# Kernel optimization log

Hardware: AMD Instinct MI355X
Metric: run time of the kernel (lower is better)

Reference implementation:

```python
import jax, jax.numpy as jnp
import numpy as np

H = 8  # n_heads from init_kwargs
EPS = 1e-5


def _ln(x, g, b):
    m = jnp.mean(x, axis=-1, keepdims=True)
    v = jnp.mean((x - m) ** 2, axis=-1, keepdims=True)
    return (x - m) * jax.lax.rsqrt(v + EPS) * g + b


def setup_inputs() -> dict:
    key = jax.random.key(0)
    B, d_m, n, L, p_d = 1, 256, 128, 1024, 128
    ks = jax.random.split(key, 12)
    s = 0.02
    return {
        "msa": jax.random.normal(ks[0], (B, d_m, n, L), jnp.float32),
        "pairs": jax.random.normal(ks[1], (B, n, n, p_d), jnp.float32),
        "ln_m_g": jnp.ones((d_m,), jnp.float32),
        "ln_m_b": jnp.zeros((d_m,), jnp.float32),
        "ln_p_g": jnp.ones((p_d,), jnp.float32),
        "ln_p_b": jnp.zeros((p_d,), jnp.float32),
        "Wq": jax.random.normal(ks[2], (d_m, d_m), jnp.float32) * s,
        "Wk": jax.random.normal(ks[3], (d_m, d_m), jnp.float32) * s,
        "Wv": jax.random.normal(ks[4], (d_m, d_m), jnp.float32) * s,
        "Wg": jax.random.normal(ks[5], (d_m, d_m), jnp.float32) * s,
        "bg": jnp.zeros((d_m,), jnp.float32),
        "Wb": jax.random.normal(ks[6], (p_d, H), jnp.float32) * s,
        "Wo": jax.random.normal(ks[7], (d_m, d_m), jnp.float32) * s,
        "bo": jnp.zeros((d_m,), jnp.float32),
    }


def reference(msa, pairs, ln_m_g, ln_m_b, ln_p_g, ln_p_b,
              Wq, Wk, Wv, Wg, bg, Wb, Wo, bo):
    B, d_m, n, L = msa.shape
    dh = d_m // H
    sqrt_c = jnp.sqrt(jnp.asarray(dh, msa.dtype))

    x = _ln(jnp.transpose(msa, (0, 3, 2, 1)), ln_m_g, ln_m_b)      # [B,L,n,d_m]
    p = _ln(pairs, ln_p_g, ln_p_b)                                   # [B,n,n,p_d]

    # pair bias: (B,n,n,H) -> (B,1,H,n_q,n_k)
    bias = jnp.transpose(jnp.einsum('bijc,ch->bijh', p, Wb), (0, 3, 1, 2))[:, None]

    def heads(y):  # [B,L,n,d_m] -> [B,L,H,n,dh]
        return jnp.transpose(y.reshape(B, L, n, H, dh), (0, 1, 3, 2, 4))

    q = heads(x @ Wq)
    k = heads(x @ Wk)
    v = heads(x @ Wv)
    g = jax.nn.sigmoid(heads(x @ Wg + bg))

    scores = jnp.einsum('blhnd,blhmd->blhnm', q, k) / sqrt_c + bias  # [B,L,H,n,n]
    w = jax.nn.softmax(scores, axis=-1)
    attn = g * jnp.einsum('blhnm,blhmd->blhnd', w, v)                # [B,L,H,n,dh]

    attn = jnp.transpose(attn, (0, 1, 3, 2, 4)).reshape(B, L, n, d_m)
    out = attn @ Wo + bo                                             # [B,L,n,d_m]
    return jnp.transpose(out, (0, 3, 2, 1))                          # [B,d_m,n,L]
```

## Files before the change

### kernel.cpp

```cpp
#include <hip/hip_runtime.h>

__device__ __forceinline__ float bf1(unsigned short s){ return __uint_as_float((unsigned)s << 16); }
__device__ __forceinline__ unsigned short f2bf(float f){
  unsigned u = __float_as_uint(f);
  u += 0x7fffu + ((u >> 16) & 1u);
  return (unsigned short)(u >> 16);
}
__device__ __forceinline__ unsigned cvt_pk_bf16(float a, float b){
  unsigned r;
  asm("v_cvt_pk_bf16_f32 %0, %1, %2" : "=v"(r) : "v"(a), "v"(b));
  return r;
}

typedef __attribute__((ext_vector_type(8))) short short8;
typedef __attribute__((ext_vector_type(4))) float f32x4;

__device__ __forceinline__ f32x4 mfma16(short8 a, short8 b, f32x4 c){
  return __builtin_amdgcn_mfma_f32_16x16x32_bf16(a, b, c, 0, 0, 0);
}

#define GLOAD_LDS16(g, l) \
  __builtin_amdgcn_global_load_lds((const __attribute__((address_space(1))) unsigned int*)(g), \
                                   (__attribute__((address_space(3))) unsigned int*)(l), 16, 0, 0)

__global__ __launch_bounds__(256) void ln_msa_kernel(
    const float* __restrict__ msa, const float* __restrict__ gam,
    const float* __restrict__ bet, unsigned short* __restrict__ x16)
{
  __shared__ float tile[256*33];
  __shared__ float ps[8*32], pq[8*32];
  __shared__ float mean_s[32], rstd_s[32];
  const int t = threadIdx.x;
  const int l0 = blockIdx.x * 32;
  const int n  = blockIdx.y;
  {
    const int lt = t & 31, ct = t >> 5;
    for (int r = 0; r < 32; ++r) {
      int c = r*8 + ct;
      tile[c*33 + lt] = msa[(size_t)c*131072 + (size_t)n*1024 + l0 + lt];
    }
  }
  __syncthreads();
  {
    const int lt = t & 31, cp = t >> 5;
    float s1 = 0.f, s2 = 0.f;
    for (int cc = 0; cc < 32; ++cc) {
      int c = cp*32 + ((cc + cp*4) & 31);
      float v = tile[c*33 + lt];
      s1 += v; s2 += v*v;
    }
    ps[cp*32 + lt] = s1; pq[cp*32 + lt] = s2;
  }
  __syncthreads();
  if (t < 32) {
    float s1 = 0.f, s2 = 0.f;
    for (int cp = 0; cp < 8; ++cp){ s1 += ps[cp*32+t]; s2 += pq[cp*32+t]; }
    float m = s1 * (1.f/256.f);
    float v = s2 * (1.f/256.f) - m*m;
    mean_s[t] = m;
    rstd_s[t] = rsqrtf(v + 1e-5f);
  }
  __syncthreads();
  {
    const float g = gam[t], b = bet[t];
    for (int l = 0; l < 32; ++l) {
      float v = (tile[t*33 + l] - mean_s[l]) * rstd_s[l] * g + b;
      x16[((size_t)(l0+l)*128 + n)*256 + t] = f2bf(v);
    }
  }
}

__global__ __launch_bounds__(64) void pair_bias_kernel(
    const float* __restrict__ pairs, const float* __restrict__ gam,
    const float* __restrict__ bet, const float* __restrict__ Wb,
    float* __restrict__ biasb)
{
  const int j = blockIdx.x, i = blockIdx.y;
  const int t = threadIdx.x;
  const float* row = pairs + ((size_t)i*128 + j)*128;
  float v0 = row[t], v1 = row[t+64];
  float s = v0 + v1;
  #pragma unroll
  for (int o = 1; o < 64; o <<= 1) s += __shfl_xor(s, o, 64);
  float m = s * (1.f/128.f);
  float d0 = v0 - m, d1 = v1 - m;
  float q = d0*d0 + d1*d1;
  #pragma unroll
  for (int o = 1; o < 64; o <<= 1) q += __shfl_xor(q, o, 64);
  float rstd = rsqrtf(q * (1.f/128.f) + 1e-5f);
  float n0 = d0 * rstd * gam[t]    + bet[t];
  float n1 = d1 * rstd * gam[t+64] + bet[t+64];
  #pragma unroll
  for (int h = 0; h < 8; ++h) {
    float p = n0 * Wb[t*8 + h] + n1 * Wb[(t+64)*8 + h];
    #pragma unroll
    for (int o = 1; o < 64; o <<= 1) p += __shfl_xor(p, o, 64);
    if (t == h) biasb[((size_t)h*128 + i)*128 + j] = p;
  }
}

__global__ __launch_bounds__(256) void wprep_kernel(
    const float* __restrict__ Wq, const float* __restrict__ Wk,
    const float* __restrict__ Wv, const float* __restrict__ Wg,
    const float* __restrict__ Wo,
    unsigned short* __restrict__ Wt, unsigned short* __restrict__ WoT)
{
  const int n = blockIdx.x, k = threadIdx.x;
  if (n < 1024) {
    const int mat = n >> 8, nl = n & 255;
    const float* W = (mat==0) ? Wq : (mat==1) ? Wk : (mat==2) ? Wv : Wg;
    float v = W[(size_t)k*256 + nl];
    if (mat == 0) v *= 0.17677669529663689f;
    Wt[(size_t)n*256 + k] = f2bf(v);
  } else {
    const int c = n - 1024;
    WoT[(size_t)c*256 + k] = f2bf(Wo[(size_t)k*256 + c]);
  }
}

__global__ __launch_bounds__(512) void fused_qkvg_attn(
    const unsigned short* __restrict__ X, const unsigned short* __restrict__ Wt,
    const float* __restrict__ bg, const float* __restrict__ biasb,
    unsigned short* __restrict__ attn2)
{
  __shared__ __align__(16) unsigned short lds[81920];
  unsigned short* Xs  = lds;
  unsigned short* Wst = lds + 32768;
  unsigned short* qs  = lds + 65536;
  unsigned short* ks  = lds + 69632;
  unsigned short* vs  = lds + 73728;
  unsigned short* gs  = lds + 77824;

  const int t = threadIdx.x, l = blockIdx.x;
  const int w = t>>6, fr = t&15, quad = (t>>4)&3;
  const int mat = w>>1, dh = (w&1)*16;
  const int d0 = dh + quad*4;
  unsigned short* pw = Wst + w*2176;
  const int rbase = w*16;
  const f32x4 zero4 = {0.f,0.f,0.f,0.f};

  #pragma unroll
  for (int s = 0; s < 8; ++s) {
    int cid = s*512 + t;
    int k0b = cid>>10, r = (cid>>3)&127, pch = cid&7;
    int c = pch ^ (r&7);
    const unsigned short* g = X + ((size_t)l*128 + r)*256 + k0b*64 + c*8;
    GLOAD_LDS16(g, Xs + (cid & ~63)*8);
  }

  for (int h = 0; h < 8; ++h) {
    #pragma unroll
    for (int s = 0; s < 8; ++s) {
      int cid = s*512 + t;
      int k0b = cid>>10, r = (cid>>3)&127, pch = cid&7;
      int c = pch ^ (r&7);
      const unsigned short* g = Wt + ((size_t)((r>>5)*256 + h*32 + (r&31)))*256 + k0b*64 + c*8;
      GLOAD_LDS16(g, Wst + (cid & ~63)*8);
    }
    __syncthreads();

    f32x4 acc[8] = {};
    for (int k0 = 0; k0 < 4; ++k0) {
      #pragma unroll
      for (int kt = 0; kt < 2; ++kt) {
        const int ck = kt*4 + quad;
        const int lr = mat*32 + dh + fr;
        short8 bf = *(const short8*)(Wst + k0*8192 + lr*64 + (ck^(lr&7))*8);
        #pragma unroll
        for (int mt = 0; mt < 8; ++mt) {
          const int r = mt*16 + fr;
          short8 af = *(const short8*)(Xs + k0*8192 + r*64 + (ck^(r&7))*8);
          acc[mt] = mfma16(bf, af, acc[mt]);
        }
      }
    }

    if (mat == 2) {
      #pragma unroll
      for (int mt = 0; mt < 8; ++mt) {
        const int m = mt*16 + fr;
        #pragma unroll
        for (int reg = 0; reg < 4; ++reg) {
          const int d = d0 + reg;
          vs[d*128 + (((m>>3)^(d&7))<<3) + (m&7)] = f2bf(acc[mt][reg]);
        }
      }
    } else {
      unsigned short* buf = (mat==0) ? qs : (mat==1) ? ks : gs;
      float4 b4;
      if (mat == 3) b4 = *(const float4*)(bg + h*32 + d0);
      #pragma unroll
      for (int mt = 0; mt < 8; ++mt) {
        const int m = mt*16 + fr;
        float v0 = acc[mt][0], v1 = acc[mt][1], v2 = acc[mt][2], v3 = acc[mt][3];
        if (mat == 3) {
          v0 = 1.f/(1.f + __expf(-(v0 + b4.x)));
          v1 = 1.f/(1.f + __expf(-(v1 + b4.y)));
          v2 = 1.f/(1.f + __expf(-(v2 + b4.z)));
          v3 = 1.f/(1.f + __expf(-(v3 + b4.w)));
        }
        uint2 pk;
        pk.x = cvt_pk_bf16(v0, v1);
        pk.y = cvt_pk_bf16(v2, v3);
        *(uint2*)(buf + m*32 + d0) = pk;
      }
    }
    __syncthreads();

    short8 aq = *(const short8*)(qs + (rbase+fr)*32 + quad*8);
    f32x4 S[8];
    #pragma unroll
    for (int nt=0;nt<8;++nt) {
      short8 bk = *(const short8*)(ks + (nt*16+fr)*32 + quad*8);
      S[nt] = mfma16(aq, bk, zero4);
    }
    const float* bb = biasb + ((size_t)h*128 + rbase + quad*4)*128 + fr;
    #pragma unroll
    for (int nt=0;nt<8;++nt)
      #pragma unroll
      for (int reg=0;reg<4;++reg)
        S[nt][reg] += bb[(size_t)reg*128 + nt*16];
    float mx[4] = {-1e30f,-1e30f,-1e30f,-1e30f};
    #pragma unroll
    for (int nt=0;nt<8;++nt)
      #pragma unroll
      for (int reg=0;reg<4;++reg) mx[reg] = fmaxf(mx[reg], S[nt][reg]);
    #pragma unroll
    for (int reg=0;reg<4;++reg) {
      mx[reg] = fmaxf(mx[reg], __shfl_xor(mx[reg], 1, 64));
      mx[reg] = fmaxf(mx[reg], __shfl_xor(mx[reg], 2, 64));
      mx[reg] = fmaxf(mx[reg], __shfl_xor(mx[reg], 4, 64));
      mx[reg] = fmaxf(mx[reg], __shfl_xor(mx[reg], 8, 64));
    }
    float sum[4] = {0.f,0.f,0.f,0.f};
    #pragma unroll
    for (int nt=0;nt<8;++nt)
      #pragma unroll
      for (int reg=0;reg<4;++reg) {
        float e = __expf(S[nt][reg]-mx[reg]);
        S[nt][reg] = e; sum[reg] += e;
      }
    #pragma unroll
    for (int reg=0;reg<4;++reg) {
      sum[reg] += __shfl_xor(sum[reg], 1, 64);
      sum[reg] += __shfl_xor(sum[reg], 2, 64);
      sum[reg] += __shfl_xor(sum[reg], 4, 64);
      sum[reg] += __shfl_xor(sum[reg], 8, 64);
    }
    float inv[4];
    #pragma unroll
    for (int reg=0;reg<4;++reg) inv[reg] = 1.f/sum[reg];
    #pragma unroll
    for (int nt=0;nt<8;++nt)
      #pragma unroll
      for (int reg=0;reg<4;++reg)
        pw[(quad*4+reg)*136 + nt*16 + fr] = f2bf(S[nt][reg]*inv[reg]);
    __builtin_amdgcn_s_waitcnt(0);
    f32x4 o[2] = {zero4, zero4};
    #pragma unroll
    for (int kt=0;kt<4;++kt) {
      short8 ap = *(const short8*)(pw + fr*136 + kt*32 + quad*8);
      #pragma unroll
      for (int n2=0;n2<2;++n2) {
        const int d = n2*16 + fr;
        const int ph = (kt*4+quad) ^ (d&7);
        short8 bv = *(const short8*)(vs + d*128 + ph*8);
        o[n2] = mfma16(ap, bv, o[n2]);
      }
    }
    #pragma unroll
    for (int n2=0;n2<2;++n2)
      #pragma unroll
      for (int reg=0;reg<4;++reg) {
        const int row = rbase + quad*4 + reg, col = n2*16 + fr;
        const float gv = bf1(gs[row*32 + col]);
        attn2[((size_t)row*1024 + l)*256 + h*32 + col] = f2bf(o[n2][reg]*gv);
      }
    __syncthreads();
  }
}

__global__ __launch_bounds__(256) void outproj_mfma(
    const unsigned short* __restrict__ attn2, const unsigned short* __restrict__ WoT,
    const float* __restrict__ bo, float* __restrict__ out)
{
  __shared__ __align__(16) unsigned short As[128*64], Bs[128*64];
  const int t = threadIdx.x;
  const int c0 = blockIdx.x*128;
  const int l0 = blockIdx.y*128;
  const int n  = blockIdx.z;
  const int w = t>>6, lane = t&63, fr = lane&15, quad = lane>>4;
  const int wm = (w>>1)*64, wn = (w&1)*64;
  f32x4 acc[4][4] = {};
  for (int k0 = 0; k0 < 256; k0 += 64) {
    if (k0) __syncthreads();
    #pragma unroll
    for (int pss = 0; pss < 4; ++pss) {
      int s = pss*256 + t;
      int row = s >> 3, pch = s & 7;
      int c = pch ^ (row & 7);
      const unsigned short* ga = WoT   + (size_t)(c0+row)*256 + k0 + c*8;
      const unsigned short* gb = attn2 + ((size_t)n*1024 + l0 + row)*256 + k0 + c*8;
      GLOAD_LDS16(ga, As + (s & ~63)*8);
      GLOAD_LDS16(gb, Bs + (s & ~63)*8);
    }
    __syncthreads();
    #pragma unroll
    for (int kt = 0; kt < 2; ++kt) {
      short8 af[4], bfr[4];
      #pragma unroll
      for (int mt=0;mt<4;++mt){ int r = wm+mt*16+fr; int ch = (kt*4+quad)^(r&7);
        af[mt] = *(const short8*)(As + r*64 + ch*8); }
      #pragma unroll
      for (int nt=0;nt<4;++nt){ int r = wn+nt*16+fr; int ch = (kt*4+quad)^(r&7);
        bfr[nt] = *(const short8*)(Bs + r*64 + ch*8); }
      #pragma unroll
      for (int mt=0;mt<4;++mt)
        #pragma unroll
        for (int nt=0;nt<4;++nt)
          acc[mt][nt] = mfma16(af[mt], bfr[nt], acc[mt][nt]);
    }
  }
  #pragma unroll
  for (int mt=0;mt<4;++mt) {
    #pragma unroll
    for (int reg=0;reg<4;++reg) {
      const int c = c0 + wm + mt*16 + quad*4 + reg;
      const float bv = bo[c];
      #pragma unroll
      for (int nt=0;nt<4;++nt) {
        const int l = l0 + wn + nt*16 + fr;
        out[(size_t)c*131072 + (size_t)n*1024 + l] = acc[mt][nt][reg] + bv;
      }
    }
  }
}

extern "C" void kernel_launch(void* const* d_in, const int* in_sizes, int n_in,
                              void* d_out, int out_size, void* d_ws, size_t ws_size,
                              hipStream_t stream) {
  const float* msa    = (const float*)d_in[0];
  const float* pairs  = (const float*)d_in[1];
  const float* ln_m_g = (const float*)d_in[2];
  const float* ln_m_b = (const float*)d_in[3];
  const float* ln_p_g = (const float*)d_in[4];
  const float* ln_p_b = (const float*)d_in[5];
  const float* Wq     = (const float*)d_in[6];
  const float* Wk     = (const float*)d_in[7];
  const float* Wv     = (const float*)d_in[8];
  const float* Wg     = (const float*)d_in[9];
  const float* bg     = (const float*)d_in[10];
  const float* Wb     = (const float*)d_in[11];
  const float* Wo     = (const float*)d_in[12];
  const float* bo     = (const float*)d_in[13];
  float* out = (float*)d_out;

  char* ws = (char*)d_ws;
  unsigned short* attn2= (unsigned short*)(ws);
  unsigned short* x16  = (unsigned short*)(ws + (size_t)268435456);
  float*          biasb= (float*)         (ws + (size_t)335544320);
  unsigned short* Wt   = (unsigned short*)(ws + (size_t)336068608);
  unsigned short* WoT  = (unsigned short*)(ws + (size_t)336592896);

  hipLaunchKernelGGL(ln_msa_kernel, dim3(32,128), dim3(256), 0, stream,
                     msa, ln_m_g, ln_m_b, x16);
  hipLaunchKernelGGL(pair_bias_kernel, dim3(128,128), dim3(64), 0, stream,
                     pairs, ln_p_g, ln_p_b, Wb, biasb);
  hipLaunchKernelGGL(wprep_kernel, dim3(1280), dim3(256), 0, stream,
                     Wq, Wk, Wv, Wg, Wo, Wt, WoT);
  hipLaunchKernelGGL(fused_qkvg_attn, dim3(1024), dim3(512), 0, stream,
                     x16, Wt, bg, biasb, attn2);
  hipLaunchKernelGGL(outproj_mfma, dim3(2,8,128), dim3(256), 0, stream,
                     attn2, WoT, bo, out);
}
```

Measured before the change: 554.9 us.

## Keep per-wave projection weights in registers with next-head prefetch; pad q/k/g/v LDS

Each wave now loads only its own weight fragments for the QKVG projection straight from global memory into registers, instead of staging the whole per-head weight tile through LDS. The next head's fragments are prefetched after the projection MFMAs so the load overlaps the epilogue and attention phases. The q/k/g row stride is padded to 40 and the v row stride to 136 to reduce LDS bank conflicts. The wait before the PV step now waits only on lgkmcnt rather than all counters. This shrinks LDS use and removes a staging pass, at the cost of more vector registers held live across the loop.

Measured after the change: 591.6 us. 6.6% more time.

```diff
diff --git a/kernel.cpp b/kernel.cpp
--- a/kernel.cpp
+++ b/kernel.cpp
@@ -118,24 +118,26 @@
   }
 }
 
+#define QP 40
+#define VP 136
 __global__ __launch_bounds__(512) void fused_qkvg_attn(
     const unsigned short* __restrict__ X, const unsigned short* __restrict__ Wt,
     const float* __restrict__ bg, const float* __restrict__ biasb,
     unsigned short* __restrict__ attn2)
 {
-  __shared__ __align__(16) unsigned short lds[81920];
+  __shared__ __align__(16) unsigned short lds[69888];
   unsigned short* Xs  = lds;
-  unsigned short* Wst = lds + 32768;
-  unsigned short* qs  = lds + 65536;
-  unsigned short* ks  = lds + 69632;
-  unsigned short* vs  = lds + 73728;
-  unsigned short* gs  = lds + 77824;
+  unsigned short* qs  = lds + 32768;
+  unsigned short* ks  = lds + 37888;
+  unsigned short* gs  = lds + 43008;
+  unsigned short* vs  = lds + 48128;
+  unsigned short* pbuf= lds + 52480;
 
   const int t = threadIdx.x, l = blockIdx.x;
   const int w = t>>6, fr = t&15, quad = (t>>4)&3;
   const int mat = w>>1, dh = (w&1)*16;
   const int d0 = dh + quad*4;
-  unsigned short* pw = Wst + w*2176;
+  unsigned short* pw = pbuf + w*2176;
   const int rbase = w*16;
   const f32x4 zero4 = {0.f,0.f,0.f,0.f};
 
@@ -148,24 +150,22 @@
     GLOAD_LDS16(g, Xs + (cid & ~63)*8);
   }
 
+  const unsigned short* wptr = Wt + ((size_t)(mat*256 + dh + fr))*256 + quad*8;
+  short8 wreg[8];
+  #pragma unroll
+  for (int i = 0; i < 8; ++i)
+    wreg[i] = *(const short8*)(wptr + (i>>1)*64 + (i&1)*32);
+
   for (int h = 0; h < 8; ++h) {
-    #pragma unroll
-    for (int s = 0; s < 8; ++s) {
-      int cid = s*512 + t;
-      int k0b = cid>>10, r = (cid>>3)&127, pch = cid&7;
-      int c = pch ^ (r&7);
-      const unsigned short* g = Wt + ((size_t)((r>>5)*256 + h*32 + (r&31)))*256 + k0b*64 + c*8;
-      GLOAD_LDS16(g, Wst + (cid & ~63)*8);
-    }
     __syncthreads();
 
     f32x4 acc[8] = {};
+    #pragma unroll
     for (int k0 = 0; k0 < 4; ++k0) {
       #pragma unroll
       for (int kt = 0; kt < 2; ++kt) {
         const int ck = kt*4 + quad;
-        const int lr = mat*32 + dh + fr;
-        short8 bf = *(const short8*)(Wst + k0*8192 + lr*64 + (ck^(lr&7))*8);
+        const short8 bf = wreg[k0*2 + kt];
         #pragma unroll
         for (int mt = 0; mt < 8; ++mt) {
           const int r = mt*16 + fr;
@@ -175,6 +175,13 @@
       }
     }
 
+    if (h < 7) {
+      const unsigned short* wn = wptr + (size_t)(h+1)*8192;
+      #pragma unroll
+      for (int i = 0; i < 8; ++i)
+        wreg[i] = *(const short8*)(wn + (i>>1)*64 + (i&1)*32);
+    }
+
     if (mat == 2) {
       #pragma unroll
       for (int mt = 0; mt < 8; ++mt) {
@@ -182,7 +189,7 @@
         #pragma unroll
         for (int reg = 0; reg < 4; ++reg) {
           const int d = d0 + reg;
-          vs[d*128 + (((m>>3)^(d&7))<<3) + (m&7)] = f2bf(acc[mt][reg]);
+          vs[d*VP + (((m>>3)^(d&7))<<3) + (m&7)] = f2bf(acc[mt][reg]);
         }
       }
     } else {
@@ -202,16 +209,16 @@
         uint2 pk;
         pk.x = cvt_pk_bf16(v0, v1);
         pk.y = cvt_pk_bf16(v2, v3);
-        *(uint2*)(buf + m*32 + d0) = pk;
+        *(uint2*)(buf + m*QP + d0) = pk;
       }
     }
     __syncthreads();
 
-    short8 aq = *(const short8*)(qs + (rbase+fr)*32 + quad*8);
+    short8 aq = *(const short8*)(qs + (rbase+fr)*QP + quad*8);
     f32x4 S[8];
     #pragma unroll
     for (int nt=0;nt<8;++nt) {
-      short8 bk = *(const short8*)(ks + (nt*16+fr)*32 + quad*8);
+      short8 bk = *(const short8*)(ks + (nt*16+fr)*QP + quad*8);
       S[nt] = mfma16(aq, bk, zero4);
     }
     const float* bb = biasb + ((size_t)h*128 + rbase + quad*4)*128 + fr;
@@ -255,7 +262,7 @@
       #pragma unroll
       for (int reg=0;reg<4;++reg)
         pw[(quad*4+reg)*136 + nt*16 + fr] = f2bf(S[nt][reg]*inv[reg]);
-    __builtin_amdgcn_s_waitcnt(0);
+    asm volatile("s_waitcnt lgkmcnt(0)" ::: "memory");
     f32x4 o[2] = {zero4, zero4};
     #pragma unroll
     for (int kt=0;kt<4;++kt) {
@@ -264,7 +271,7 @@
       for (int n2=0;n2<2;++n2) {
         const int d = n2*16 + fr;
         const int ph = (kt*4+quad) ^ (d&7);
-        short8 bv = *(const short8*)(vs + d*128 + ph*8);
+        short8 bv = *(const short8*)(vs + d*VP + ph*8);
         o[n2] = mfma16(ap, bv, o[n2]);
       }
     }
@@ -273,7 +280,7 @@
       #pragma unroll
       for (int reg=0;reg<4;++reg) {
         const int row = rbase + quad*4 + reg, col = n2*16 + fr;
-        const float gv = bf1(gs[row*32 + col]);
+        const float gv = bf1(gs[row*QP + col]);
         attn2[((size_t)row*1024 + l)*256 + h*32 + col] = f2bf(o[n2][reg]*gv);
       }
     __syncthreads();
```

## Swizzle q/k/g LDS layout and stage outproj epilogue through LDS

Applied to the files above, without the earlier changes.

Applies an XOR swizzle to the 32-wide q/k/g LDS rows in the attention kernel so the 16-byte fragment reads used by the MFMA loads hit fewer bank conflicts. The output-projection epilogue is rewritten to stage accumulators in shared memory one 64-channel half at a time, then write out 128-bit vectors along the contiguous L axis. Before, each store was a scattered scalar fp32 write. This adds extra barriers and LDS traffic in exchange for coalesced global writes.

Measured after the change: 554.7 us. Within noise of the previous version (-0.0%).

```diff
diff --git a/kernel.cpp b/kernel.cpp
--- a/kernel.cpp
+++ b/kernel.cpp
@@ -138,6 +138,7 @@
   unsigned short* pw = Wst + w*2176;
   const int rbase = w*16;
   const f32x4 zero4 = {0.f,0.f,0.f,0.f};
+  const int frsw = (fr>>1)&3;
 
   #pragma unroll
   for (int s = 0; s < 8; ++s) {
@@ -202,16 +203,16 @@
         uint2 pk;
         pk.x = cvt_pk_bf16(v0, v1);
         pk.y = cvt_pk_bf16(v2, v3);
-        *(uint2*)(buf + m*32 + d0) = pk;
-      }
-    }
-    __syncthreads();
-
-    short8 aq = *(const short8*)(qs + (rbase+fr)*32 + quad*8);
+        *(uint2*)(buf + m*32 + ((((d0>>3) ^ ((m>>1)&3))<<3)) + (d0&7)) = pk;
+      }
+    }
+    __syncthreads();
+
+    short8 aq = *(const short8*)(qs + (rbase+fr)*32 + ((quad ^ frsw)<<3));
     f32x4 S[8];
     #pragma unroll
     for (int nt=0;nt<8;++nt) {
-      short8 bk = *(const short8*)(ks + (nt*16+fr)*32 + quad*8);
+      short8 bk = *(const short8*)(ks + (nt*16+fr)*32 + ((quad ^ frsw)<<3));
       S[nt] = mfma16(aq, bk, zero4);
     }
     const float* bb = biasb + ((size_t)h*128 + rbase + quad*4)*128 + fr;
@@ -273,7 +274,8 @@
       #pragma unroll
       for (int reg=0;reg<4;++reg) {
         const int row = rbase + quad*4 + reg, col = n2*16 + fr;
-        const float gv = bf1(gs[row*32 + col]);
+        const int rsw = ((quad*4+reg)>>1)&3;
+        const float gv = bf1(gs[row*32 + ((((n2*2)+(fr>>3)) ^ rsw)<<3) + (fr&7)]);
         attn2[((size_t)row*1024 + l)*256 + h*32 + col] = f2bf(o[n2][reg]*gv);
       }
     __syncthreads();
@@ -284,7 +286,9 @@
     const unsigned short* __restrict__ attn2, const unsigned short* __restrict__ WoT,
     const float* __restrict__ bo, float* __restrict__ out)
 {
-  __shared__ __align__(16) unsigned short As[128*64], Bs[128*64];
+  __shared__ __align__(16) unsigned short sm[2*128*64];
+  unsigned short* As = sm;
+  unsigned short* Bs = sm + 128*64;
   const int t = threadIdx.x;
   const int c0 = blockIdx.x*128;
   const int l0 = blockIdx.y*128;
@@ -321,18 +325,40 @@
           acc[mt][nt] = mfma16(af[mt], bfr[nt], acc[mt][nt]);
     }
   }
+  __syncthreads();
+  float* ob = (float*)sm;
+  const int hw = w >> 1;
   #pragma unroll
-  for (int mt=0;mt<4;++mt) {
-    #pragma unroll
-    for (int reg=0;reg<4;++reg) {
-      const int c = c0 + wm + mt*16 + quad*4 + reg;
+  for (int half = 0; half < 2; ++half) {
+    if (hw == half) {
+      #pragma unroll
+      for (int mt=0;mt<4;++mt)
+        #pragma unroll
+        for (int nt=0;nt<4;++nt)
+          #pragma unroll
+          for (int reg=0;reg<4;++reg) {
+            const int cl = mt*16 + quad*4 + reg;
+            const int ll = wn + nt*16 + fr;
+            ob[cl*128 + ll] = acc[mt][nt][reg];
+          }
+    }
+    __syncthreads();
+    #pragma unroll
+    for (int p = 0; p < 4; ++p) {
+      const int id = p*256 + t;
+      const int cl = id >> 4, l8 = (id & 15)*8;
+      const float4 a = *(const float4*)(ob + cl*128 + l8);
+      const float4 b = *(const float4*)(ob + cl*128 + l8 + 4);
+      const int c = c0 + half*64 + cl;
       const float bv = bo[c];
-      #pragma unroll
-      for (int nt=0;nt<4;++nt) {
-        const int l = l0 + wn + nt*16 + fr;
-        out[(size_t)c*131072 + (size_t)n*1024 + l] = acc[mt][nt][reg] + bv;
-      }
-    }
+      float4 sa = a, sb = b;
+      sa.x += bv; sa.y += bv; sa.z += bv; sa.w += bv;
+      sb.x += bv; sb.y += bv; sb.z += bv; sb.w += bv;
+      float* op = out + (size_t)c*131072 + (size_t)n*1024 + l0 + l8;
+      *(float4*)op = sa;
+      *(float4*)(op+4) = sb;
+    }
+    __syncthreads();
   }
 }
 
```
